# Optimization experiments

Hardware: AMD Instinct MI355X
Metric: run time of the kernel (lower is better)

## Reference

```python
import jax, jax.numpy as jnp
import numpy as np

SCALE = 0.08838834764831845  # 1/sqrt(head_size=128)
NEG_INF = -1e9


def setup_inputs() -> dict:
    key = jax.random.key(0)
    ks = jax.random.split(key, 8)
    NH, HS = 32, 128                 # heads, head_size
    NP, NS, G = 2048, 4, 64          # prompt tokens, prompt seqs, decode tokens
    NT = NP + G                      # total valid tokens
    NB, BS, MB = 1024, 16, 32        # num cache blocks, block_size, max blocks/seq
    q = jax.random.normal(ks[0], (NT, NH * HS), jnp.float32)
    k = jax.random.normal(ks[1], (NT, NH * HS), jnp.float32)
    v = jax.random.normal(ks[2], (NT, NH * HS), jnp.float32)
    kc = jax.random.normal(ks[3], (NB, NH, HS, BS), jnp.float32)
    vc = jax.random.normal(ks[4], (NB, NH, HS, BS), jnp.float32)
    bt = jax.random.randint(ks[5], (G, MB), 0, NB, jnp.int32)
    cl = jax.random.randint(ks[6], (G,), 1, MB * BS + 1, jnp.int32)  # >=1 so softmax is defined
    sm = jax.random.randint(ks[7], (NT,), 0, NB * BS, jnp.int32)
    return {"query": q, "key": k, "value": v, "key_cache": kc, "value_cache": vc,
            "block_tables": bt, "context_lens": cl, "slot_mapping": sm,
            "num_prompt_tokens": NP, "num_prompt_seqs": NS}


def reference(query, key, value, key_cache, value_cache, block_tables,
              context_lens, slot_mapping, num_prompt_tokens, num_prompt_seqs):
    NB, NH, HS, BS = key_cache.shape
    q = query.reshape(-1, NH, HS)
    k = key.reshape(-1, NH, HS)
    v = value.reshape(-1, NH, HS)
    NP, NS = num_prompt_tokens, num_prompt_seqs
    L = NP // NS  # equal-length prompts -> block-diagonal causal == batched causal

    # --- prompt phase: multi-query causal MHA (xformers path) ---
    qp = q[:NP].reshape(NS, L, NH, HS)
    kp = k[:NP].reshape(NS, L, NH, HS)
    vp = v[:NP].reshape(NS, L, NH, HS)
    scores = jnp.einsum('bqhd,bkhd->bhqk', qp, kp) * SCALE
    causal = jnp.tril(jnp.ones((L, L), bool))
    scores = jnp.where(causal, scores, NEG_INF)
    probs = jax.nn.softmax(scores, axis=-1)
    out_p = jnp.einsum('bhqk,bkhd->bqhd', probs, vp).reshape(NP, NH, HS)

    # --- reshape_and_cache: scatter all valid tokens' K/V into paged cache ---
    blk = slot_mapping // BS
    off = slot_mapping % BS
    key_cache = key_cache.at[blk, :, :, off].set(k)
    value_cache = value_cache.at[blk, :, :, off].set(v)

    # --- decode phase: single-query paged attention over block tables ---
    qd = q[NP:]                                  # [G, NH, HS]
    G, MB = block_tables.shape
    # gather blocks: [G, MB, NH, HS, BS] -> [G, MB*BS, NH, HS]
    kd = jnp.transpose(key_cache[block_tables], (0, 1, 4, 2, 3)).reshape(G, MB * BS, NH, HS)
    vd = jnp.transpose(value_cache[block_tables], (0, 1, 4, 2, 3)).reshape(G, MB * BS, NH, HS)
    sc = jnp.einsum('ghd,gkhd->ghk', qd, kd) * SCALE
    valid = jnp.arange(MB * BS)[None, :] < context_lens[:, None]   # [G, K]
    sc = jnp.where(valid[:, None, :], sc, NEG_INF)
    pd = jax.nn.softmax(sc, axis=-1)
    out_d = jnp.einsum('ghk,gkhd->ghd', pd, vd)

    out = jnp.concatenate([out_p, out_d], axis=0)
    return out.reshape(-1, NH * HS)
```

## Files before the change

### kernel.cpp

```cpp
#include <hip/hip_runtime.h>
#include <stdint.h>

#define NH    32
#define HS    128
#define NPT   2048
#define NT    2112
#define NBLK  1024
#define BS    16
#define MBMAX 32
#define LSEQ  512
#define DMODEL 4096
#define SCALE 0.08838834764831845f

typedef __bf16 bf16x8 __attribute__((ext_vector_type(8)));
typedef float  f32x4  __attribute__((ext_vector_type(4)));

__device__ __forceinline__ unsigned short f2bf(float f) {
    unsigned u = __float_as_uint(f);
    u += 0x7fffu + ((u >> 16) & 1u);
    return (unsigned short)(u >> 16);
}
__device__ __forceinline__ unsigned pack2(float a, float b) {
    return (unsigned)f2bf(a) | ((unsigned)f2bf(b) << 16);
}
__device__ __forceinline__ float sel4(const float a[4], int i) {
    float r = a[0];
    r = (i == 1) ? a[1] : r;
    r = (i == 2) ? a[2] : r;
    r = (i == 3) ? a[3] : r;
    return r;
}

__global__ void init_winner(int* __restrict__ w) {
    int i = blockIdx.x * 256 + threadIdx.x;
    if (i < NBLK * BS) w[i] = -1;
}
__global__ void fill_winner(const int* __restrict__ sm, int* __restrict__ w) {
    int t = blockIdx.x * 256 + threadIdx.x;
    if (t < NT) atomicMax(&w[sm[t]], t);
}

#define QKS 136
__device__ __forceinline__ int vtidx(int d, int t) {
    return d * 72 + (t ^ (((d >> 3) & 3) * 8));
}

__global__ __launch_bounds__(256, 2) void prompt_attn(
    const float* __restrict__ q, const float* __restrict__ k,
    const float* __restrict__ v, float* __restrict__ out) {

    __shared__ __align__(16) unsigned short Qs[64 * QKS];
    __shared__ __align__(16) unsigned short Ks[64 * QKS];
    __shared__ __align__(16) unsigned short Vt[128 * 72 + 32];
    __shared__ __align__(16) unsigned short Ps[4 * 16 * 72];

    const int tid  = threadIdx.x;
    const int lane = tid & 63, wq = tid >> 6;
    const int quad = lane >> 4, m15 = lane & 15;
    const int qt = 7 - (blockIdx.x & 7);
    const int h  = (blockIdx.x >> 3) & 31;
    const int s  = blockIdx.x >> 8;
    const int qbase  = s * LSEQ + qt * 64;
    const int kbase0 = s * LSEQ;

    {
        const int r0 = tid >> 5, c4 = (tid & 31) * 4;
        #pragma unroll
        for (int p = 0; p < 8; ++p) {
            int r = r0 + p * 8;
            float4 t = *(const float4*)(q + (size_t)(qbase + r) * DMODEL + h * HS + c4);
            uint2 w; w.x = pack2(t.x * SCALE, t.y * SCALE); w.y = pack2(t.z * SCALE, t.w * SCALE);
            *(uint2*)(&Qs[r * QKS + c4]) = w;
        }
    }

    f32x4 O[8];
    #pragma unroll
    for (int i = 0; i < 8; ++i) O[i] = (f32x4){0.f, 0.f, 0.f, 0.f};
    float mrun[4], lrun[4];
    #pragma unroll
    for (int r = 0; r < 4; ++r) { mrun[r] = -1e30f; lrun[r] = 0.f; }

    unsigned short* Pw = Ps + wq * (16 * 72);

    for (int kt = 0; kt <= qt; ++kt) {
        {
            const int r0 = tid >> 5, c4 = (tid & 31) * 4;
            #pragma unroll
            for (int p = 0; p < 8; ++p) {
                int r = r0 + p * 8;
                float4 t = *(const float4*)(k + (size_t)(kbase0 + kt * 64 + r) * DMODEL + h * HS + c4);
                uint2 w; w.x = pack2(t.x, t.y); w.y = pack2(t.z, t.w);
                *(uint2*)(&Ks[r * QKS + c4]) = w;
            }
        }
        {
            const int g = tid >> 2, sub = tid & 3;
            const int lbase = lane & ~3;
            #pragma unroll
            for (int p = 0; p < 8; ++p) {
                const int tb = (p & 3) * 16, db = (p >> 2) * 64;
                const int tok  = tb + (g >> 4) * 4 + sub;
                const int dim4 = db + (g & 15) * 4;
                float4 t = *(const float4*)(v + (size_t)(kbase0 + kt * 64 + tok) * DMODEL + h * HS + dim4);
                float in[4] = {t.x, t.y, t.z, t.w};
                float rec[4];
                #pragma unroll
                for (int r = 0; r < 4; ++r) {
                    float pub = sel4(in, (sub + 4 - r) & 3);
                    rec[r] = __shfl(pub, lbase + ((sub + r) & 3));
                }
                float o4[4];
                #pragma unroll
                for (int j = 0; j < 4; ++j) o4[j] = sel4(rec, (j + 4 - sub) & 3);
                const int d  = dim4 + sub;
                const int t0 = tb + (g >> 4) * 4;
                uint2 w2; w2.x = pack2(o4[0], o4[1]); w2.y = pack2(o4[2], o4[3]);
                *(uint2*)(&Vt[vtidx(d, t0)]) = w2;
            }
        }
        __syncthreads();

        bf16x8 aq[4];
        #pragma unroll
        for (int kc = 0; kc < 4; ++kc)
            aq[kc] = *(const bf16x8*)(&Qs[(wq * 16 + m15) * QKS + kc * 32 + quad * 8]);
        f32x4 S[4];
        #pragma unroll
        for (int nt = 0; nt < 4; ++nt) {
            S[nt] = (f32x4){0.f, 0.f, 0.f, 0.f};
            #pragma unroll
            for (int kc = 0; kc < 4; ++kc) {
                bf16x8 bk = *(const bf16x8*)(&Ks[(nt * 16 + m15) * QKS + kc * 32 + quad * 8]);
                S[nt] = __builtin_amdgcn_mfma_f32_16x16x32_bf16(aq[kc], bk, S[nt], 0, 0, 0);
            }
        }
        if (kt == qt) {
            #pragma unroll
            for (int nt = 0; nt < 4; ++nt) {
                const int C = nt * 16 + m15;
                #pragma unroll
                for (int reg = 0; reg < 4; ++reg) {
                    const int R = wq * 16 + quad * 4 + reg;
                    if (C > R) S[nt][reg] = -1e30f;
                }
            }
        }

        #pragma unroll
        for (int reg = 0; reg < 4; ++reg) {
            float x = fmaxf(fmaxf(S[0][reg], S[1][reg]), fmaxf(S[2][reg], S[3][reg]));
            x = fmaxf(x, __shfl_xor(x, 1));
            x = fmaxf(x, __shfl_xor(x, 2));
            x = fmaxf(x, __shfl_xor(x, 4));
            x = fmaxf(x, __shfl_xor(x, 8));
            const float mn = fmaxf(mrun[reg], x);
            const float al = __expf(mrun[reg] - mn);
            mrun[reg] = mn;
            float sum = 0.f;
            #pragma unroll
            for (int nt = 0; nt < 4; ++nt) {
                float pv = __expf(S[nt][reg] - mn);
                S[nt][reg] = pv;
                sum += pv;
            }
            sum += __shfl_xor(sum, 1);
            sum += __shfl_xor(sum, 2);
            sum += __shfl_xor(sum, 4);
            sum += __shfl_xor(sum, 8);
            lrun[reg] = lrun[reg] * al + sum;
            #pragma unroll
            for (int n2 = 0; n2 < 8; ++n2) O[n2][reg] *= al;
        }

        #pragma unroll
        for (int nt = 0; nt < 4; ++nt) {
            #pragma unroll
            for (int reg = 0; reg < 4; ++reg) {
                float v0 = S[nt][reg];
                float v1 = __shfl_xor(v0, 1);
                if (!(lane & 1))
                    *(unsigned*)(&Pw[(quad * 4 + reg) * 72 + nt * 16 + m15]) = pack2(v0, v1);
            }
        }

        bf16x8 ap[2];
        #pragma unroll
        for (int kc = 0; kc < 2; ++kc)
            ap[kc] = *(const bf16x8*)(&Pw[m15 * 72 + kc * 32 + quad * 8]);
        #pragma unroll
        for (int n2 = 0; n2 < 8; ++n2) {
            #pragma unroll
            for (int kc = 0; kc < 2; ++kc) {
                bf16x8 bv = *(const bf16x8*)(&Vt[vtidx(n2 * 16 + m15, kc * 32 + quad * 8)]);
                O[n2] = __builtin_amdgcn_mfma_f32_16x16x32_bf16(ap[kc], bv, O[n2], 0, 0, 0);
            }
        }
        __syncthreads();
    }

    float inv[4];
    #pragma unroll
    for (int reg = 0; reg < 4; ++reg) inv[reg] = 1.f / lrun[reg];
    #pragma unroll
    for (int n2 = 0; n2 < 8; ++n2) {
        #pragma unroll
        for (int reg = 0; reg < 4; ++reg) {
            out[(size_t)(qbase + wq * 16 + quad * 4 + reg) * DMODEL + h * HS + n2 * 16 + m15] =
                O[n2][reg] * inv[reg];
        }
    }
}

__global__ __launch_bounds__(256, 3) void decode_attn(
    const float* __restrict__ q, const float* __restrict__ k, const float* __restrict__ v,
    const float* __restrict__ kcache, const float* __restrict__ vcache,
    const int* __restrict__ bt, const int* __restrict__ cl,
    const int* __restrict__ winner, float* __restrict__ out) {

    __shared__ float pm[4], pl[4];
    __shared__ float pacc[4][128];

    const int tid = threadIdx.x, w = tid >> 6, lane = tid & 63;
    const int g = blockIdx.x >> 5, h = blockIdx.x & 31;
    const int n  = cl[g];
    const int nb = (n + 15) >> 4;

    const int p4 = lane >> 2;
    const int ob = (lane & 3) * 4;

    const float* qp = q + (size_t)(NPT + g) * DMODEL + h * HS;
    float qreg[8];
    #pragma unroll
    for (int i = 0; i < 8; ++i) qreg[i] = qp[p4 + 16 * i] * SCALE;

    float m = -1e30f, l = 0.f;
    float acc[8];
    #pragma unroll
    for (int i = 0; i < 8; ++i) acc[i] = 0.f;

    f32x4 kv[8], vv[8];
    int blk = 0;
    if (w < nb) {
        blk = bt[g * MBMAX + w];
        const float* kb = kcache + ((size_t)blk * NH + h) * (HS * BS);
        #pragma unroll
        for (int i = 0; i < 8; ++i)
            kv[i] = *(const f32x4*)(kb + lane * 4 + i * 256);
    }

    for (int jb = w; jb < nb; jb += 4) {
        const float* vb = vcache + ((size_t)blk * NH + h) * (HS * BS);
        #pragma unroll
        for (int i = 0; i < 8; ++i)
            vv[i] = *(const f32x4*)(vb + lane * 4 + i * 256);

        const int4 wt4 = *(const int4*)(winner + blk * BS + ob);
        const int wtj[4] = {wt4.x, wt4.y, wt4.z, wt4.w};
        const bool anyw = __any(wt4.x >= 0 || wt4.y >= 0 || wt4.z >= 0 || wt4.w >= 0);

        if (anyw) {
            #pragma unroll
            for (int j = 0; j < 4; ++j) {
                if (wtj[j] >= 0) {
                    const float* fr = k + (size_t)wtj[j] * DMODEL + h * HS + p4;
                    #pragma unroll
                    for (int i = 0; i < 8; ++i) kv[i][j] = fr[16 * i];
                }
            }
        }

        float s[4];
        #pragma unroll
        for (int j = 0; j < 4; ++j) s[j] = 0.f;
        #pragma unroll
        for (int i = 0; i < 8; ++i) {
            s[0] += qreg[i] * kv[i][0];
            s[1] += qreg[i] * kv[i][1];
            s[2] += qreg[i] * kv[i][2];
            s[3] += qreg[i] * kv[i][3];
        }
        #pragma unroll
        for (int j = 0; j < 4; ++j) {
            s[j] += __shfl_xor(s[j], 4);
            s[j] += __shfl_xor(s[j], 8);
            s[j] += __shfl_xor(s[j], 16);
            s[j] += __shfl_xor(s[j], 32);
            if (jb * 16 + ob + j >= n) s[j] = -1e30f;
        }

        float tm = fmaxf(fmaxf(s[0], s[1]), fmaxf(s[2], s[3]));
        tm = fmaxf(tm, __shfl_xor(tm, 1));
        tm = fmaxf(tm, __shfl_xor(tm, 2));
        const float mn = fmaxf(m, tm);
        const float al = __expf(m - mn);
        m = mn;
        float p[4], ps = 0.f;
        #pragma unroll
        for (int j = 0; j < 4; ++j) { p[j] = __expf(s[j] - mn); ps += p[j]; }
        ps += __shfl_xor(ps, 1);
        ps += __shfl_xor(ps, 2);
        l = l * al + ps;
        #pragma unroll
        for (int i = 0; i < 8; ++i) acc[i] *= al;

        const int jn = jb + 4;
        if (jn < nb) {
            blk = bt[g * MBMAX + jn];
            const float* kb = kcache + ((size_t)blk * NH + h) * (HS * BS);
            #pragma unroll
            for (int i = 0; i < 8; ++i)
                kv[i] = *(const f32x4*)(kb + lane * 4 + i * 256);
        }

        if (anyw) {
            #pragma unroll
            for (int j = 0; j < 4; ++j) {
                if (wtj[j] >= 0) {
                    const float* fr = v + (size_t)wtj[j] * DMODEL + h * HS + p4;
                    #pragma unroll
                    for (int i = 0; i < 8; ++i) vv[i][j] = fr[16 * i];
                }
            }
        }
        #pragma unroll
        for (int i = 0; i < 8; ++i)
            acc[i] += p[0] * vv[i][0] + p[1] * vv[i][1]
                    + p[2] * vv[i][2] + p[3] * vv[i][3];
    }

    #pragma unroll
    for (int i = 0; i < 8; ++i) {
        acc[i] += __shfl_xor(acc[i], 1);
        acc[i] += __shfl_xor(acc[i], 2);
    }
    if (lane == 0) { pm[w] = m; pl[w] = l; }
    if ((lane & 3) == 0) {
        #pragma unroll
        for (int i = 0; i < 8; ++i) pacc[w][p4 + 16 * i] = acc[i];
    }
    __syncthreads();
    if (tid < 128) {
        const float M = fmaxf(fmaxf(pm[0], pm[1]), fmaxf(pm[2], pm[3]));
        float L = 0.f, A = 0.f;
        #pragma unroll
        for (int w2 = 0; w2 < 4; ++w2) {
            const float e = __expf(pm[w2] - M);
            L += e * pl[w2];
            A += e * pacc[w2][tid];
        }
        out[(size_t)(NPT + g) * DMODEL + h * HS + tid] = A / L;
    }
}

extern "C" void kernel_launch(void* const* d_in, const int* in_sizes, int n_in,
                              void* d_out, int out_size, void* d_ws, size_t ws_size,
                              hipStream_t stream) {
    const float* q  = (const float*)d_in[0];
    const float* k  = (const float*)d_in[1];
    const float* v  = (const float*)d_in[2];
    const float* kc = (const float*)d_in[3];
    const float* vc = (const float*)d_in[4];
    const int* bt   = (const int*)d_in[5];
    const int* cl   = (const int*)d_in[6];
    const int* sm   = (const int*)d_in[7];
    float* out  = (float*)d_out;
    int* winner = (int*)d_ws;

    hipLaunchKernelGGL(init_winner, dim3(64),   dim3(256), 0, stream, winner);
    hipLaunchKernelGGL(fill_winner, dim3(9),    dim3(256), 0, stream, sm, winner);
    hipLaunchKernelGGL(prompt_attn, dim3(1024), dim3(256), 0, stream, q, k, v, out);
    hipLaunchKernelGGL(decode_attn, dim3(2048), dim3(256), 0, stream,
                       q, k, v, kc, vc, bt, cl, winner, out);
}
```

Measured before the change: 694.7 us.

## Prefetch next K/V tile into registers, load Q fragments directly, memset winner

The prompt attention kernel now loads the next 64-token K and V tile from global memory into registers while the current tile's MFMA work runs, so global load latency overlaps with compute. Q fragments are read straight from global into MFMA operand registers, which removes the Q shared-memory buffer and the per-iteration LDS reads. The init_winner kernel is replaced by hipMemsetAsync. The register prefetch adds 64 VGPRs of float4 state, which may hurt occupancy under launch_bounds(256,2) or cause spills.

```diff
diff --git a/kernel.cpp b/kernel.cpp
--- a/kernel.cpp
+++ b/kernel.cpp
@@ -31,10 +31,6 @@
     return r;
 }
 
-__global__ void init_winner(int* __restrict__ w) {
-    int i = blockIdx.x * 256 + threadIdx.x;
-    if (i < NBLK * BS) w[i] = -1;
-}
 __global__ void fill_winner(const int* __restrict__ sm, int* __restrict__ w) {
     int t = blockIdx.x * 256 + threadIdx.x;
     if (t < NT) atomicMax(&w[sm[t]], t);
@@ -49,7 +45,6 @@
     const float* __restrict__ q, const float* __restrict__ k,
     const float* __restrict__ v, float* __restrict__ out) {
 
-    __shared__ __align__(16) unsigned short Qs[64 * QKS];
     __shared__ __align__(16) unsigned short Ks[64 * QKS];
     __shared__ __align__(16) unsigned short Vt[128 * 72 + 32];
     __shared__ __align__(16) unsigned short Ps[4 * 16 * 72];
@@ -63,68 +58,94 @@
     const int qbase  = s * LSEQ + qt * 64;
     const int kbase0 = s * LSEQ;
 
+    bf16x8 aq[4];
     {
-        const int r0 = tid >> 5, c4 = (tid & 31) * 4;
+        const float* qr = q + (size_t)(qbase + wq * 16 + m15) * DMODEL + h * HS + quad * 8;
+        #pragma unroll
+        for (int kc = 0; kc < 4; ++kc) {
+            float4 t0 = *(const float4*)(qr + kc * 32);
+            float4 t1 = *(const float4*)(qr + kc * 32 + 4);
+            union { unsigned u[4]; bf16x8 v; } cv;
+            cv.u[0] = pack2(t0.x * SCALE, t0.y * SCALE);
+            cv.u[1] = pack2(t0.z * SCALE, t0.w * SCALE);
+            cv.u[2] = pack2(t1.x * SCALE, t1.y * SCALE);
+            cv.u[3] = pack2(t1.z * SCALE, t1.w * SCALE);
+            aq[kc] = cv.v;
+        }
+    }
+
+    f32x4 O[8];
+    #pragma unroll
+    for (int i = 0; i < 8; ++i) O[i] = (f32x4){0.f, 0.f, 0.f, 0.f};
+    float mrun[4], lrun[4];
+    #pragma unroll
+    for (int r = 0; r < 4; ++r) { mrun[r] = -1e30f; lrun[r] = 0.f; }
+
+    unsigned short* Pw = Ps + wq * (16 * 72);
+
+    const int r0 = tid >> 5, c4 = (tid & 31) * 4;
+    const int gv = tid >> 2, sub = tid & 3;
+    const int lbase = lane & ~3;
+
+    float4 kreg[8], vreg[8];
+    #pragma unroll
+    for (int p = 0; p < 8; ++p) {
+        int r = r0 + p * 8;
+        kreg[p] = *(const float4*)(k + (size_t)(kbase0 + r) * DMODEL + h * HS + c4);
+    }
+    #pragma unroll
+    for (int p = 0; p < 8; ++p) {
+        const int tb = (p & 3) * 16, db = (p >> 2) * 64;
+        const int tok  = tb + (gv >> 4) * 4 + sub;
+        const int dim4 = db + (gv & 15) * 4;
+        vreg[p] = *(const float4*)(v + (size_t)(kbase0 + tok) * DMODEL + h * HS + dim4);
+    }
+
+    for (int kt = 0; kt <= qt; ++kt) {
         #pragma unroll
         for (int p = 0; p < 8; ++p) {
             int r = r0 + p * 8;
-            float4 t = *(const float4*)(q + (size_t)(qbase + r) * DMODEL + h * HS + c4);
-            uint2 w; w.x = pack2(t.x * SCALE, t.y * SCALE); w.y = pack2(t.z * SCALE, t.w * SCALE);
-            *(uint2*)(&Qs[r * QKS + c4]) = w;
-        }
-    }
-
-    f32x4 O[8];
-    #pragma unroll
-    for (int i = 0; i < 8; ++i) O[i] = (f32x4){0.f, 0.f, 0.f, 0.f};
-    float mrun[4], lrun[4];
-    #pragma unroll
-    for (int r = 0; r < 4; ++r) { mrun[r] = -1e30f; lrun[r] = 0.f; }
-
-    unsigned short* Pw = Ps + wq * (16 * 72);
-
-    for (int kt = 0; kt <= qt; ++kt) {
-        {
-            const int r0 = tid >> 5, c4 = (tid & 31) * 4;
+            float4 t = kreg[p];
+            uint2 w; w.x = pack2(t.x, t.y); w.y = pack2(t.z, t.w);
+            *(uint2*)(&Ks[r * QKS + c4]) = w;
+        }
+        #pragma unroll
+        for (int p = 0; p < 8; ++p) {
+            const int tb = (p & 3) * 16, db = (p >> 2) * 64;
+            const int dim4 = db + (gv & 15) * 4;
+            float4 t = vreg[p];
+            float in[4] = {t.x, t.y, t.z, t.w};
+            float rec[4];
+            #pragma unroll
+            for (int r = 0; r < 4; ++r) {
+                float pub = sel4(in, (sub + 4 - r) & 3);
+                rec[r] = __shfl(pub, lbase + ((sub + r) & 3));
+            }
+            float o4[4];
+            #pragma unroll
+            for (int j = 0; j < 4; ++j) o4[j] = sel4(rec, (j + 4 - sub) & 3);
+            const int d  = dim4 + sub;
+            const int t0 = tb + (gv >> 4) * 4;
+            uint2 w2; w2.x = pack2(o4[0], o4[1]); w2.y = pack2(o4[2], o4[3]);
+            *(uint2*)(&Vt[vtidx(d, t0)]) = w2;
+        }
+        __syncthreads();
+
+        if (kt < qt) {
             #pragma unroll
             for (int p = 0; p < 8; ++p) {
                 int r = r0 + p * 8;
-                float4 t = *(const float4*)(k + (size_t)(kbase0 + kt * 64 + r) * DMODEL + h * HS + c4);
-                uint2 w; w.x = pack2(t.x, t.y); w.y = pack2(t.z, t.w);
-                *(uint2*)(&Ks[r * QKS + c4]) = w;
-            }
-        }
-        {
-            const int g = tid >> 2, sub = tid & 3;
-            const int lbase = lane & ~3;
+                kreg[p] = *(const float4*)(k + (size_t)(kbase0 + (kt + 1) * 64 + r) * DMODEL + h * HS + c4);
+            }
             #pragma unroll
             for (int p = 0; p < 8; ++p) {
                 const int tb = (p & 3) * 16, db = (p >> 2) * 64;
-                const int tok  = tb + (g >> 4) * 4 + sub;
-                const int dim4 = db + (g & 15) * 4;
-                float4 t = *(const float4*)(v + (size_t)(kbase0 + kt * 64 + tok) * DMODEL + h * HS + dim4);
-                float in[4] = {t.x, t.y, t.z, t.w};
-                float rec[4];
-                #pragma unroll
-                for (int r = 0; r < 4; ++r) {
-                    float pub = sel4(in, (sub + 4 - r) & 3);
-                    rec[r] = __shfl(pub, lbase + ((sub + r) & 3));
-                }
-                float o4[4];
-                #pragma unroll
-                for (int j = 0; j < 4; ++j) o4[j] = sel4(rec, (j + 4 - sub) & 3);
-                const int d  = dim4 + sub;
-                const int t0 = tb + (g >> 4) * 4;
-                uint2 w2; w2.x = pack2(o4[0], o4[1]); w2.y = pack2(o4[2], o4[3]);
-                *(uint2*)(&Vt[vtidx(d, t0)]) = w2;
-            }
-        }
-        __syncthreads();
-
-        bf16x8 aq[4];
-        #pragma unroll
-        for (int kc = 0; kc < 4; ++kc)
-            aq[kc] = *(const bf16x8*)(&Qs[(wq * 16 + m15) * QKS + kc * 32 + quad * 8]);
+                const int tok  = tb + (gv >> 4) * 4 + sub;
+                const int dim4 = db + (gv & 15) * 4;
+                vreg[p] = *(const float4*)(v + (size_t)(kbase0 + (kt + 1) * 64 + tok) * DMODEL + h * HS + dim4);
+            }
+        }
+
         f32x4 S[4];
         #pragma unroll
         for (int nt = 0; nt < 4; ++nt) {
@@ -367,7 +388,7 @@
     float* out  = (float*)d_out;
     int* winner = (int*)d_ws;
 
-    hipLaunchKernelGGL(init_winner, dim3(64),   dim3(256), 0, stream, winner);
+    hipMemsetAsync(winner, 0xFF, (size_t)NBLK * BS * sizeof(int), stream);
     hipLaunchKernelGGL(fill_winner, dim3(9),    dim3(256), 0, stream, sm, winner);
     hipLaunchKernelGGL(prompt_attn, dim3(1024), dim3(256), 0, stream, q, k, v, out);
     hipLaunchKernelGGL(decode_attn, dim3(2048), dim3(256), 0, stream,
```

Result: slower. 708.8 us (+2.0%).
